# Performance work log

Hardware: AMD Instinct MI355X
Metric: run time of the kernel (lower is better)

The kernel has to match this reference:

```python
import jax, jax.numpy as jnp
import numpy as np

H = 2048          # hidden size
NH = 32           # query heads
NKV = 8           # kv heads
HD = H // NH      # head dim = 64
GROUPS = NH // NKV
S = 2048          # seq len
B = 1
SCALE = HD ** -0.5


def _rope_tables(seq, dim, base=10000.0):
    inv = 1.0 / (base ** (np.arange(0, dim, 2, dtype=np.float32) / dim))
    t = np.arange(seq, dtype=np.float32)
    freqs = np.outer(t, inv)                     # [S, dim/2]
    emb = np.concatenate([freqs, freqs], axis=-1)  # [S, dim]
    return jnp.asarray(np.cos(emb)), jnp.asarray(np.sin(emb))


def setup_inputs() -> dict:
    key = jax.random.key(0)
    ks = jax.random.split(key, 5)
    x = jax.random.normal(ks[0], (B, S, H), dtype=jnp.float32)
    wq = jax.random.normal(ks[1], (H, NH * HD), dtype=jnp.float32) * (H ** -0.5)
    wk = jax.random.normal(ks[2], (H, NKV * HD), dtype=jnp.float32) * (H ** -0.5)
    wv = jax.random.normal(ks[3], (H, NKV * HD), dtype=jnp.float32) * (H ** -0.5)
    wo = jax.random.normal(ks[4], (NH * HD, H), dtype=jnp.float32) * (H ** -0.5)
    cos, sin = _rope_tables(S, HD)
    mask = jnp.tril(jnp.ones((S, S), dtype=bool))[None, None]  # causal [1,1,S,S]
    return {"x": x, "wq": wq, "wk": wk, "wv": wv, "wo": wo,
            "cos": cos, "sin": sin, "mask": mask}


def _rotate_half(t):
    t1, t2 = jnp.split(t, 2, axis=-1)
    return jnp.concatenate([-t2, t1], axis=-1)


def reference(x, wq, wk, wv, wo, cos, sin, mask):
    b, s, _ = x.shape
    # projections
    q = (x @ wq).reshape(b, s, NH, HD).transpose(0, 2, 1, 3)    # [B,NH,S,HD]
    k = (x @ wk).reshape(b, s, NKV, HD).transpose(0, 2, 1, 3)   # [B,NKV,S,HD]
    v = (x @ wv).reshape(b, s, NKV, HD).transpose(0, 2, 1, 3)
    # RoPE (cos/sin broadcast over batch and heads)
    c = cos[None, None]; sn = sin[None, None]
    q = q * c + _rotate_half(q) * sn
    k = k * c + _rotate_half(k) * sn
    # GQA: repeat kv heads to match query heads
    k = jnp.repeat(k, GROUPS, axis=1)                           # [B,NH,S,HD]
    v = jnp.repeat(v, GROUPS, axis=1)
    # scores + causal mask + softmax (dropout p=0 -> identity in eval)
    scores = SCALE * jnp.einsum('bhqd,bhkd->bhqk', q, k)
    scores = jnp.where(mask, scores, -jnp.inf)
    attn = jax.nn.softmax(scores, axis=-1)
    out = jnp.einsum('bhqk,bhkd->bhqd', attn, v)
    out = out.transpose(0, 2, 1, 3).reshape(b, s, NH * HD)
    return out @ wo
```

## Files before the change

### kernel.cpp

```cpp
#include <hip/hip_runtime.h>

typedef unsigned short u16;
typedef unsigned u32;
typedef u16 u16x8 __attribute__((ext_vector_type(8)));
typedef u16 u16x4 __attribute__((ext_vector_type(4)));
typedef u32 u32x4 __attribute__((ext_vector_type(4)));
typedef __bf16 bf8 __attribute__((ext_vector_type(8)));
typedef float f32x4 __attribute__((ext_vector_type(4)));
typedef float f32x16 __attribute__((ext_vector_type(16)));

__device__ __forceinline__ u16 f2b(float f) {
  unsigned u = __float_as_uint(f);
  u += 0x7FFFu + ((u >> 16) & 1u);
  return (u16)(u >> 16);
}
__device__ __forceinline__ float b2f(u16 h) {
  return __uint_as_float(((unsigned)h) << 16);
}
__device__ __forceinline__ bf8 asbf8(u16x8 v) {
  return __builtin_bit_cast(bf8, v);
}
__device__ __forceinline__ void gll16(const u16* g, u16* l) {
  __builtin_amdgcn_global_load_lds(
      (const __attribute__((address_space(1))) unsigned*)(g),
      (__attribute__((address_space(3))) unsigned*)(l), 16, 0, 0);
}
__device__ __forceinline__ u32 cvtpk(float lo, float hi) {
  u32 r;
  asm("v_cvt_pk_bf16_f32 %0, %1, %2" : "=v"(r) : "v"(lo), "v"(hi));
  return r;
}
__device__ __forceinline__ void plswap(u32& a, u32& b) {
  asm("v_permlane32_swap_b32 %0, %1" : "+v"(a), "+v"(b));
}
__device__ __forceinline__ float ex2(float x) {
  return __builtin_amdgcn_exp2f(x);
}
#define MFMA32(A,B,C) __builtin_amdgcn_mfma_f32_32x32x16_bf16(A,B,C,0,0,0)


__global__ __launch_bounds__(256) void xconv(const float* __restrict__ x,
                                             u16* __restrict__ xb) {
  int i = (blockIdx.x * 256 + threadIdx.x) * 4;
  float4 v = *(const float4*)(x + i);
  u16x4 o;
  o[0] = f2b(v.x); o[1] = f2b(v.y); o[2] = f2b(v.z); o[3] = f2b(v.w);
  *(u16x4*)(xb + i) = o;
}

__global__ __launch_bounds__(256) void wtrans(const float* __restrict__ in,
                                              u16* __restrict__ out,
                                              int N, int K) {
  __shared__ float tile[32][33];
  int tx = threadIdx.x & 31, ty = threadIdx.x >> 5;
  int n0 = blockIdx.x * 32, k0 = blockIdx.y * 32;
#pragma unroll
  for (int yy = 0; yy < 32; yy += 8)
    tile[ty + yy][tx] = in[(size_t)(k0 + ty + yy) * N + n0 + tx];
  __syncthreads();
#pragma unroll
  for (int yy = 0; yy < 32; yy += 8)
    out[(size_t)(n0 + ty + yy) * K + k0 + tx] = f2b(tile[tx][ty + yy]);
}

__global__ __launch_bounds__(256) void reduce_qkv(u16* __restrict__ p0,
                                                  const u16* __restrict__ p1,
                                                  const float* __restrict__ cs,
                                                  const float* __restrict__ sn) {
  int idx = blockIdx.x * 256 + threadIdx.x;
  int s = idx / 384, c8 = (idx % 384) * 8;
  size_t base = (size_t)s * 3072 + c8;
  if (c8 < 2560) {
    int hc = c8 & 63;
    if (hc >= 32) return;
    u16x8 a0 = *(const u16x8*)(p0 + base);
    u16x8 a1 = *(const u16x8*)(p1 + base);
    u16x8 b0 = *(const u16x8*)(p0 + base + 32);
    u16x8 b1 = *(const u16x8*)(p1 + base + 32);
    u16x8 oa, ob;
#pragma unroll
    for (int e = 0; e < 8; ++e) {
      float va = b2f(a0[e]) + b2f(a1[e]);
      float vb = b2f(b0[e]) + b2f(b1[e]);
      float c1 = cs[s * 64 + hc + e],      s1 = sn[s * 64 + hc + e];
      float c2 = cs[s * 64 + hc + 32 + e], s2 = sn[s * 64 + hc + 32 + e];
      oa[e] = f2b(va * c1 - vb * s1);
      ob[e] = f2b(vb * c2 + va * s2);
    }
    *(u16x8*)(p0 + base)      = oa;
    *(u16x8*)(p0 + base + 32) = ob;
  } else {
    u16x8 a0 = *(const u16x8*)(p0 + base);
    u16x8 a1 = *(const u16x8*)(p1 + base);
    u16x8 o;
#pragma unroll
    for (int e = 0; e < 8; ++e) o[e] = f2b(b2f(a0[e]) + b2f(a1[e]));
    *(u16x8*)(p0 + base) = o;
  }
}

__global__ __launch_bounds__(256) void reduce_out(const u16* __restrict__ p0,
                                                  const u16* __restrict__ p1,
                                                  float* __restrict__ out) {
  int idx = blockIdx.x * 256 + threadIdx.x;
  size_t base = (size_t)idx * 8;
  u16x8 a0 = *(const u16x8*)(p0 + base);
  u16x8 a1 = *(const u16x8*)(p1 + base);
  float4 lo, hi;
  lo.x = b2f(a0[0]) + b2f(a1[0]); lo.y = b2f(a0[1]) + b2f(a1[1]);
  lo.z = b2f(a0[2]) + b2f(a1[2]); lo.w = b2f(a0[3]) + b2f(a1[3]);
  hi.x = b2f(a0[4]) + b2f(a1[4]); hi.y = b2f(a0[5]) + b2f(a1[5]);
  hi.z = b2f(a0[6]) + b2f(a1[6]); hi.w = b2f(a0[7]) + b2f(a1[7]);
  *(float4*)(out + base)     = lo;
  *(float4*)(out + base + 4) = hi;
}

__global__ __launch_bounds__(256) void ktrans_f(const u16* __restrict__ qkv,
                                                u16* __restrict__ Kf) {
  int tid = blockIdx.x * 256 + threadIdx.x;
  int s = tid >> 6, cc = tid & 63;
  int kh = cc >> 3, c = cc & 7;
  int j = c >> 1, hi = c & 1;
  int b = s >> 5, la = s & 31;
  u16x8 v = *(const u16x8*)(qkv + (size_t)s * 3072 + 2048 + cc * 8);
  *(u16x8*)(Kf + ((((size_t)(kh * 64 + b) * 4 + j) * 2 + hi) * 32 + la) * 8) = v;
}

__global__ __launch_bounds__(256) void vtrans_f(const u16* __restrict__ qkv,
                                                u16* __restrict__ Vf) {
  int tid = blockIdx.x * 256 + threadIdx.x;
  int s = tid >> 6, cc = tid & 63;
  int kh = cc >> 3, c = cc & 7;
  int m = c >> 2, laB = (c & 3) * 8;
  int b = s >> 5, s5 = s & 31;
  int jj = s5 >> 4, hi = (s5 >> 3) & 1, e = s5 & 7;
  u16x8 v = *(const u16x8*)(qkv + (size_t)s * 3072 + 2560 + cc * 8);
  u16* dst = Vf + (((size_t)(kh * 64 + b) * 4 + m * 2 + jj) * 64 + hi * 32 + laB) * 8 + e;
#pragma unroll
  for (int i = 0; i < 8; ++i) dst[i * 8] = v[i];
}


__global__ __launch_bounds__(256) void gemm_sk(const u16* __restrict__ A,
                                               const u16* __restrict__ Bt,
                                               u16* __restrict__ C0,
                                               u16* __restrict__ C1,
                                               int N, int Kfull, int KH) {
  __shared__ __align__(16) u16 As[128 * 32];
  __shared__ __align__(16) u16 Bs[128 * 32];
  const int t = threadIdx.x;
  const int lane = t & 63, wid = t >> 6;
  const int wm = (wid >> 1) * 64, wn = (wid & 1) * 64;
  const int la = lane & 15, lg = lane >> 4;
  const int m0 = blockIdx.y * 128, n0 = blockIdx.x * 128;
  const int kbeg = blockIdx.z * KH;
  u16* C = blockIdx.z ? C1 : C0;

  const int c0 = wid * 2;
  const int srow = c0 * 16 + (lane >> 2);
  const int scol = (lane & 3) * 8;
  const u16* Ap = A + (size_t)(m0 + srow) * Kfull + kbeg + scol;
  const u16* Bp = Bt + (size_t)(n0 + srow) * Kfull + kbeg + scol;
  u16* Ad0 = &As[c0 * 512];
  u16* Ad1 = &As[(c0 + 1) * 512];
  u16* Bd0 = &Bs[c0 * 512];
  u16* Bd1 = &Bs[(c0 + 1) * 512];
  const size_t rstep = (size_t)16 * Kfull;

  f32x4 acc[4][4] = {};

  for (int k0 = 0; k0 < KH; k0 += 32) {
    __syncthreads();
    gll16(Ap + k0, Ad0);
    gll16(Ap + k0 + rstep, Ad1);
    gll16(Bp + k0, Bd0);
    gll16(Bp + k0 + rstep, Bd1);
    __syncthreads();
    bf8 af[4], bfr[4];
#pragma unroll
    for (int i = 0; i < 4; ++i)
      af[i] = asbf8(*(const u16x8*)(&As[(wm + i * 16 + la) * 32 + lg * 8]));
#pragma unroll
    for (int j = 0; j < 4; ++j)
      bfr[j] = asbf8(*(const u16x8*)(&Bs[(wn + j * 16 + la) * 32 + lg * 8]));
    __builtin_amdgcn_s_setprio(1);
#pragma unroll
    for (int i = 0; i < 4; ++i)
#pragma unroll
      for (int j = 0; j < 4; ++j)
        acc[i][j] = __builtin_amdgcn_mfma_f32_16x16x32_bf16(af[i], bfr[j],
                                                            acc[i][j], 0, 0, 0);
    __builtin_amdgcn_s_setprio(0);
  }

#pragma unroll
  for (int i = 0; i < 4; ++i)
#pragma unroll
    for (int j = 0; j < 4; ++j)
#pragma unroll
      for (int r = 0; r < 4; ++r) {
        int row = m0 + wm + i * 16 + lg * 4 + r;
        int col = n0 + wn + j * 16 + la;
        C[(size_t)row * N + col] = f2b(acc[i][j][r]);
      }
}


#define LOADKV(K0,K1,K2,K3,V0,V1,V2,V3,b) do {                       \
    const u16* kp_ = kfb + (size_t)(b) * 2048;                       \
    K0 = asbf8(*(const u16x8*)(kp_));                                \
    K1 = asbf8(*(const u16x8*)(kp_ + 512));                          \
    K2 = asbf8(*(const u16x8*)(kp_ + 1024));                         \
    K3 = asbf8(*(const u16x8*)(kp_ + 1536));                         \
    const u16* vp_ = vfb + (size_t)(b) * 2048;                       \
    V0 = asbf8(*(const u16x8*)(vp_));                                \
    V1 = asbf8(*(const u16x8*)(vp_ + 512));                          \
    V2 = asbf8(*(const u16x8*)(vp_ + 1024));                         \
    V3 = asbf8(*(const u16x8*)(vp_ + 1536));                         \
  } while (0)

#define STEP(K0,K1,K2,K3,V0,V1,V2,V3,b) do {                         \
    f32x16 s = {};                                                   \
    __builtin_amdgcn_s_setprio(1);                                   \
    s = MFMA32(K0, qf0, s);                                          \
    s = MFMA32(K1, qf1, s);                                          \
    s = MFMA32(K2, qf2, s);                                          \
    s = MFMA32(K3, qf3, s);                                          \
    __builtin_amdgcn_s_setprio(0);                                   \
    if ((b) == nb - 1) {                                             \
      _Pragma("unroll") for (int r = 0; r < 16; ++r) {               \
        int kvr = (b) * 32 + (r & 3) + 8 * (r >> 2) + 4 * hi;        \
        if (kvr > q0w + la) s[r] = -1e30f;                           \
      }                                                              \
    }                                                                \
    _Pragma("unroll") for (int r = 0; r < 16; ++r)                   \
      s[r] = ex2(s[r] - 32.0f);                                      \
    float z0 = s[0] + s[1],   z1 = s[2] + s[3];                      \
    float z2 = s[4] + s[5],   z3 = s[6] + s[7];                      \
    float z4 = s[8] + s[9],   z5 = s[10] + s[11];                    \
    float z6 = s[12] + s[13], z7 = s[14] + s[15];                    \
    l_run += ((z0 + z1) + (z2 + z3)) + ((z4 + z5) + (z6 + z7));      \
    u32 c0 = cvtpk(s[0], s[1]),   c1 = cvtpk(s[2], s[3]);            \
    u32 c2 = cvtpk(s[4], s[5]),   c3 = cvtpk(s[6], s[7]);            \
    u32 c4 = cvtpk(s[8], s[9]),   c5 = cvtpk(s[10], s[11]);          \
    u32 c6 = cvtpk(s[12], s[13]), c7 = cvtpk(s[14], s[15]);          \
    plswap(c0, c2); plswap(c1, c3); plswap(c4, c6); plswap(c5, c7);  \
    u32x4 t0; t0[0] = c0; t0[1] = c1; t0[2] = c2; t0[3] = c3;        \
    u32x4 t1; t1[0] = c4; t1[1] = c5; t1[2] = c6; t1[3] = c7;        \
    bf8 pa0 = __builtin_bit_cast(bf8, t0);                           \
    bf8 pa1 = __builtin_bit_cast(bf8, t1);                           \
    __builtin_amdgcn_s_setprio(1);                                   \
    o0 = MFMA32(pa0, V0, o0);                                        \
    o0 = MFMA32(pa1, V1, o0);                                        \
    o1 = MFMA32(pa0, V2, o1);                                        \
    o1 = MFMA32(pa1, V3, o1);                                        \
    __builtin_amdgcn_s_setprio(0);                                   \
  } while (0)

__global__ __launch_bounds__(256) void attn_fwd(const u16* __restrict__ qkv,
                                                const u16* __restrict__ Kf,
                                                const u16* __restrict__ Vf,
                                                u16* __restrict__ aout) {
  const int head = blockIdx.x;
  const int qt = 63 - (int)blockIdx.y;
  const int nb = qt + 1;
  const int q0w = qt * 32;
  const int kh = head >> 2;
  const int t = threadIdx.x;
  const int w = t >> 6;
  const int lane = t & 63;
  const int la = lane & 31;
  const int hi = lane >> 5;

  __shared__ float lS[4][32];
  __shared__ __align__(16) u16 oS[4][32][72];

  const int base = nb >> 2, rem = nb & 3;
  const int cnt = base + (w < rem);
  const int start = w * base + min(w, rem);

  bf8 qf0, qf1, qf2, qf3;
  {
    const u16* qp = qkv + (size_t)(q0w + la) * 3072 + head * 64 + hi * 8;
    const float SC = 0.125f * 1.44269504088896340736f;
#define QLOAD(dst, kk) do {                                          \
      u16x8 v = *(const u16x8*)(qp + (kk) * 16);                     \
      u16x8 sv;                                                      \
      _Pragma("unroll") for (int e = 0; e < 8; ++e)                  \
        sv[e] = f2b(b2f(v[e]) * SC);                                 \
      dst = asbf8(sv);                                               \
    } while (0)
    QLOAD(qf0, 0); QLOAD(qf1, 1); QLOAD(qf2, 2); QLOAD(qf3, 3);
#undef QLOAD
  }

  const u16* kfb = Kf + (size_t)kh * 131072 + (size_t)lane * 8;
  const u16* vfb = Vf + (size_t)kh * 131072 + (size_t)lane * 8;

  f32x16 o0 = {}, o1 = {};
  float l_run = 0.f;

  bf8 kA0, kA1, kA2, kA3, vA0, vA1, vA2, vA3;
  bf8 kB0, kB1, kB2, kB3, vB0, vB1, vB2, vB3;

  if (cnt > 0) {
    int b = start;
    const int e = start + cnt;
    LOADKV(kA0, kA1, kA2, kA3, vA0, vA1, vA2, vA3, b);
    for (;;) {
      if (b + 1 < e) LOADKV(kB0, kB1, kB2, kB3, vB0, vB1, vB2, vB3, b + 1);
      STEP(kA0, kA1, kA2, kA3, vA0, vA1, vA2, vA3, b);
      ++b; if (b >= e) break;
      if (b + 1 < e) LOADKV(kA0, kA1, kA2, kA3, vA0, vA1, vA2, vA3, b + 1);
      STEP(kB0, kB1, kB2, kB3, vB0, vB1, vB2, vB3, b);
      ++b; if (b >= e) break;
    }
  }

  {
    float lt = l_run + __shfl_xor(l_run, 32);
    if (lane < 32) lS[w][lane] = lt;
#pragma unroll
    for (int r = 0; r < 16; ++r) {
      int crow = (r & 3) + 8 * (r >> 2) + 4 * hi;
      oS[w][crow][la]      = f2b(o0[r]);
      oS[w][crow][la + 32] = f2b(o1[r]);
    }
  }
  __syncthreads();

  {
    const int q = t >> 3, d0 = (t & 7) * 8;
    float lg = (lS[0][q] + lS[1][q]) + (lS[2][q] + lS[3][q]);
    float inv = 1.0f / lg;
    u16x8 p0 = *(const u16x8*)&oS[0][q][d0];
    u16x8 p1 = *(const u16x8*)&oS[1][q][d0];
    u16x8 p2 = *(const u16x8*)&oS[2][q][d0];
    u16x8 p3 = *(const u16x8*)&oS[3][q][d0];
    u16x8 outv;
#pragma unroll
    for (int j = 0; j < 8; ++j) {
      float sum = (b2f(p0[j]) + b2f(p1[j])) + (b2f(p2[j]) + b2f(p3[j]));
      outv[j] = f2b(sum * inv);
    }
    *(u16x8*)(aout + (size_t)(q0w + q) * 2048 + head * 64 + d0) = outv;
  }
}


extern "C" void kernel_launch(void* const* d_in, const int* in_sizes, int n_in,
                              void* d_out, int out_size, void* d_ws, size_t ws_size,
                              hipStream_t stream) {
  (void)in_sizes; (void)n_in; (void)out_size; (void)ws_size;
  const float* x  = (const float*)d_in[0];
  const float* wq = (const float*)d_in[1];
  const float* wk = (const float*)d_in[2];
  const float* wv = (const float*)d_in[3];
  const float* wo = (const float*)d_in[4];
  const float* cs = (const float*)d_in[5];
  const float* sn = (const float*)d_in[6];

  u16* ws    = (u16*)d_ws;
  u16* xb    = ws;
  u16* wqkvT = ws + 4194304;
  u16* qkv   = ws + 10485760;
  u16* woT   = ws + 16777216;
  u16* ext   = ws + 20971520;
  u16* Kf    = wqkvT;
  u16* Vf    = wqkvT + 1048576;
  u16* aout  = xb;
  u16* op0   = qkv;
  u16* op1   = ext;

  xconv<<<4096, 256, 0, stream>>>(x, xb);
  wtrans<<<dim3(64, 64), 256, 0, stream>>>(wq, wqkvT, 2048, 2048);
  wtrans<<<dim3(16, 64), 256, 0, stream>>>(wk, wqkvT + (size_t)2048 * 2048, 512, 2048);
  wtrans<<<dim3(16, 64), 256, 0, stream>>>(wv, wqkvT + (size_t)2560 * 2048, 512, 2048);
  wtrans<<<dim3(64, 64), 256, 0, stream>>>(wo, woT, 2048, 2048);

  gemm_sk<<<dim3(24, 16, 2), 256, 0, stream>>>(xb, wqkvT, qkv, ext, 3072, 2048, 1024);
  reduce_qkv<<<3072, 256, 0, stream>>>(qkv, ext, cs, sn);
  ktrans_f<<<512, 256, 0, stream>>>(qkv, Kf);
  vtrans_f<<<512, 256, 0, stream>>>(qkv, Vf);
  attn_fwd<<<dim3(32, 64), 256, 0, stream>>>(qkv, Kf, Vf, aout);
  gemm_sk<<<dim3(16, 16, 2), 256, 0, stream>>>(aout, woT, op0, op1, 2048, 2048, 1024);
  reduce_out<<<2048, 256, 0, stream>>>(op0, op1, (float*)d_out);
}
```

Measured before the change: 153.1 us.

## Share K/V tiles across four query tiles via LDS staging in attention

The attention kernel now processes 128 query rows per block with 8 waves (two halves of four). Each K/V block is staged once into double-buffered shared memory with global_load_lds and reused by all four query-tile waves in a half, instead of each wave streaming K/V from global memory per 32-row query tile. The KV range is split into two halves whose partial sums are combined through shared memory at the end. This cuts redundant global/L2 traffic for K/V but adds a block-wide barrier per step and causes idle waves on masked blocks.

```diff
diff --git a/kernel.cpp b/kernel.cpp
--- a/kernel.cpp
+++ b/kernel.cpp
@@ -206,20 +206,16 @@
 }
 
 
-#define LOADKV(K0,K1,K2,K3,V0,V1,V2,V3,b) do {                       \
-    const u16* kp_ = kfb + (size_t)(b) * 2048;                       \
-    K0 = asbf8(*(const u16x8*)(kp_));                                \
-    K1 = asbf8(*(const u16x8*)(kp_ + 512));                          \
-    K2 = asbf8(*(const u16x8*)(kp_ + 1024));                         \
-    K3 = asbf8(*(const u16x8*)(kp_ + 1536));                         \
-    const u16* vp_ = vfb + (size_t)(b) * 2048;                       \
-    V0 = asbf8(*(const u16x8*)(vp_));                                \
-    V1 = asbf8(*(const u16x8*)(vp_ + 512));                          \
-    V2 = asbf8(*(const u16x8*)(vp_ + 1024));                         \
-    V3 = asbf8(*(const u16x8*)(vp_ + 1536));                         \
-  } while (0)
-
-#define STEP(K0,K1,K2,K3,V0,V1,V2,V3,b) do {                         \
+#define STEPL(buf, bb) do {                                          \
+    const u16* p_ = &smem[(((h2) << 1) | (buf)) * 4096 + lane8];     \
+    bf8 K0 = asbf8(*(const u16x8*)(p_));                             \
+    bf8 K1 = asbf8(*(const u16x8*)(p_ + 512));                       \
+    bf8 K2 = asbf8(*(const u16x8*)(p_ + 1024));                      \
+    bf8 K3 = asbf8(*(const u16x8*)(p_ + 1536));                      \
+    bf8 V0 = asbf8(*(const u16x8*)(p_ + 2048));                      \
+    bf8 V1 = asbf8(*(const u16x8*)(p_ + 2560));                      \
+    bf8 V2 = asbf8(*(const u16x8*)(p_ + 3072));                      \
+    bf8 V3 = asbf8(*(const u16x8*)(p_ + 3584));                      \
     f32x16 s = {};                                                   \
     __builtin_amdgcn_s_setprio(1);                                   \
     s = MFMA32(K0, qf0, s);                                          \
@@ -227,9 +223,9 @@
     s = MFMA32(K2, qf2, s);                                          \
     s = MFMA32(K3, qf3, s);                                          \
     __builtin_amdgcn_s_setprio(0);                                   \
-    if ((b) == nb - 1) {                                             \
+    if ((bb) == kmax) {                                              \
       _Pragma("unroll") for (int r = 0; r < 16; ++r) {               \
-        int kvr = (b) * 32 + (r & 3) + 8 * (r >> 2) + 4 * hi;        \
+        int kvr = (bb) * 32 + (r & 3) + 8 * (r >> 2) + 4 * hi;       \
         if (kvr > q0w + la) s[r] = -1e30f;                           \
       }                                                              \
     }                                                                \
@@ -257,27 +253,36 @@
     __builtin_amdgcn_s_setprio(0);                                   \
   } while (0)
 
-__global__ __launch_bounds__(256) void attn_fwd(const u16* __restrict__ qkv,
-                                                const u16* __restrict__ Kf,
-                                                const u16* __restrict__ Vf,
-                                                u16* __restrict__ aout) {
+#define STG(bb, buf) do {                                            \
+    u16* d_ = &smem[((((h2) << 1) | (buf)) * 4096) + sub * 512];     \
+    gll16(Kg + (size_t)(bb) * 2048 + sub * 512 + lane8, d_);         \
+    gll16(Vg + (size_t)(bb) * 2048 + sub * 512 + lane8, d_ + 2048);  \
+  } while (0)
+
+__global__ __launch_bounds__(512, 4) void attn_fwd(const u16* __restrict__ qkv,
+                                                   const u16* __restrict__ Kf,
+                                                   const u16* __restrict__ Vf,
+                                                   u16* __restrict__ aout) {
   const int head = blockIdx.x;
-  const int qt = 63 - (int)blockIdx.y;
-  const int nb = qt + 1;
-  const int q0w = qt * 32;
+  const int qb = 15 - (int)blockIdx.y;
+  const int Q0 = qb * 128;
+  const int Kb = qb * 4;
+  const int nb = Kb + 4;
+  const int ha = nb >> 1;
   const int kh = head >> 2;
   const int t = threadIdx.x;
-  const int w = t >> 6;
-  const int lane = t & 63;
+  const int w = t >> 6, lane = t & 63;
+  const int h2 = w >> 2;
+  const int wq = w & 3;
+  const int sub = wq;
   const int la = lane & 31;
   const int hi = lane >> 5;
-
-  __shared__ float lS[4][32];
-  __shared__ __align__(16) u16 oS[4][32][72];
-
-  const int base = nb >> 2, rem = nb & 3;
-  const int cnt = base + (w < rem);
-  const int start = w * base + min(w, rem);
+  const int lane8 = lane * 8;
+  const int q0w = Q0 + 32 * wq;
+  const int kmax = Kb + wq;
+
+  __shared__ __align__(16) u16 smem[18432];
+  __shared__ float lM[8][32];
 
   bf8 qf0, qf1, qf2, qf3;
   {
@@ -294,56 +299,47 @@
 #undef QLOAD
   }
 
-  const u16* kfb = Kf + (size_t)kh * 131072 + (size_t)lane * 8;
-  const u16* vfb = Vf + (size_t)kh * 131072 + (size_t)lane * 8;
+  const u16* Kg = Kf + (size_t)kh * 131072;
+  const u16* Vg = Vf + (size_t)kh * 131072;
 
   f32x16 o0 = {}, o1 = {};
   float l_run = 0.f;
 
-  bf8 kA0, kA1, kA2, kA3, vA0, vA1, vA2, vA3;
-  bf8 kB0, kB1, kB2, kB3, vB0, vB1, vB2, vB3;
-
-  if (cnt > 0) {
-    int b = start;
-    const int e = start + cnt;
-    LOADKV(kA0, kA1, kA2, kA3, vA0, vA1, vA2, vA3, b);
-    for (;;) {
-      if (b + 1 < e) LOADKV(kB0, kB1, kB2, kB3, vB0, vB1, vB2, vB3, b + 1);
-      STEP(kA0, kA1, kA2, kA3, vA0, vA1, vA2, vA3, b);
-      ++b; if (b >= e) break;
-      if (b + 1 < e) LOADKV(kA0, kA1, kA2, kA3, vA0, vA1, vA2, vA3, b + 1);
-      STEP(kB0, kB1, kB2, kB3, vB0, vB1, vB2, vB3, b);
-      ++b; if (b >= e) break;
-    }
+  STG(h2 ? ha : 0, 0);
+  __syncthreads();
+
+  for (int i = 0; i < ha; ++i) {
+    if (i + 1 < ha) STG(h2 ? (ha + i + 1) : (i + 1), (i + 1) & 1);
+    const int bb = h2 ? (ha + i) : i;
+    if (bb <= kmax) STEPL(i & 1, bb);
+    __syncthreads();
   }
 
   {
     float lt = l_run + __shfl_xor(l_run, 32);
-    if (lane < 32) lS[w][lane] = lt;
+    if (lane < 32) lM[w][lane] = lt;
 #pragma unroll
     for (int r = 0; r < 16; ++r) {
       int crow = (r & 3) + 8 * (r >> 2) + 4 * hi;
-      oS[w][crow][la]      = f2b(o0[r]);
-      oS[w][crow][la + 32] = f2b(o1[r]);
+      smem[(w * 32 + crow) * 72 + la]      = f2b(o0[r]);
+      smem[(w * 32 + crow) * 72 + la + 32] = f2b(o1[r]);
     }
   }
   __syncthreads();
 
-  {
-    const int q = t >> 3, d0 = (t & 7) * 8;
-    float lg = (lS[0][q] + lS[1][q]) + (lS[2][q] + lS[3][q]);
-    float inv = 1.0f / lg;
-    u16x8 p0 = *(const u16x8*)&oS[0][q][d0];
-    u16x8 p1 = *(const u16x8*)&oS[1][q][d0];
-    u16x8 p2 = *(const u16x8*)&oS[2][q][d0];
-    u16x8 p3 = *(const u16x8*)&oS[3][q][d0];
+#pragma unroll
+  for (int it = 0; it < 2; ++it) {
+    const int id = t + it * 512;
+    const int q = id >> 3, d0 = (id & 7) * 8;
+    const int wA = q >> 5, crow = q & 31;
+    float inv = 1.0f / (lM[wA][crow] + lM[wA + 4][crow]);
+    u16x8 a = *(const u16x8*)&smem[((wA)     * 32 + crow) * 72 + d0];
+    u16x8 b = *(const u16x8*)&smem[((wA + 4) * 32 + crow) * 72 + d0];
     u16x8 outv;
 #pragma unroll
-    for (int j = 0; j < 8; ++j) {
-      float sum = (b2f(p0[j]) + b2f(p1[j])) + (b2f(p2[j]) + b2f(p3[j]));
-      outv[j] = f2b(sum * inv);
-    }
-    *(u16x8*)(aout + (size_t)(q0w + q) * 2048 + head * 64 + d0) = outv;
+    for (int j = 0; j < 8; ++j)
+      outv[j] = f2b((b2f(a[j]) + b2f(b[j])) * inv);
+    *(u16x8*)(aout + (size_t)(Q0 + q) * 2048 + head * 64 + d0) = outv;
   }
 }
 
@@ -382,7 +378,7 @@
   reduce_qkv<<<3072, 256, 0, stream>>>(qkv, ext, cs, sn);
   ktrans_f<<<512, 256, 0, stream>>>(qkv, Kf);
   vtrans_f<<<512, 256, 0, stream>>>(qkv, Vf);
-  attn_fwd<<<dim3(32, 64), 256, 0, stream>>>(qkv, Kf, Vf, aout);
+  attn_fwd<<<dim3(32, 16), 512, 0, stream>>>(qkv, Kf, Vf, aout);
   gemm_sk<<<dim3(16, 16, 2), 256, 0, stream>>>(aout, woT, op0, op1, 2048, 2048, 1024);
   reduce_out<<<2048, 256, 0, stream>>>(op0, op1, (float*)d_out);
 }
```

Result: no change. 151.1 us (-1.3%).
